# Kernel optimization log

Measured on AMD Instinct MI355X. Metric: run time of the kernel, lower is better.

The kernel has to match this reference:

```python
import jax, jax.numpy as jnp
import numpy as np

INPUT_DIM = 16
BLOCK_LEVELS = 17
OUT_DIM = 5  # dim_weight


def setup_inputs() -> dict:
    key = jax.random.key(0)
    ks = jax.random.split(key, 17)
    B, H, HS = 4096, 1024, 3
    s = 0.05  # keep activations bounded through stacked relu-linears
    return {
        "x": jax.random.normal(ks[0], (B, INPUT_DIM), jnp.float32),
        "Win_f": jax.random.normal(ks[1], (BLOCK_LEVELS, 96, H), jnp.float32) * s,
        "bin_f": jax.random.normal(ks[2], (BLOCK_LEVELS, H), jnp.float32) * s,
        "Win_b": jax.random.normal(ks[3], (BLOCK_LEVELS, 96, H), jnp.float32) * s,
        "bin_b": jax.random.normal(ks[4], (BLOCK_LEVELS, H), jnp.float32) * s,
        "Wblk": jax.random.normal(ks[5], (HS, H, H), jnp.float32) * (s / 2),
        "bblk": jax.random.normal(ks[6], (HS, H), jnp.float32) * s,
        "Wout_f": jax.random.normal(ks[7], (BLOCK_LEVELS, H, OUT_DIM), jnp.float32) * s,
        "bout_f": jax.random.normal(ks[8], (BLOCK_LEVELS, OUT_DIM), jnp.float32) * s,
        "Wout_b": jax.random.normal(ks[9], (BLOCK_LEVELS, H, OUT_DIM), jnp.float32) * s,
        "bout_b": jax.random.normal(ks[10], (BLOCK_LEVELS, OUT_DIM), jnp.float32) * s,
        "W1": jax.random.normal(ks[11], (OUT_DIM, OUT_DIM), jnp.float32) * s,
        "W2": jax.random.normal(ks[12], (OUT_DIM, OUT_DIM), jnp.float32) * s,
        "W3": jax.random.normal(ks[13], (OUT_DIM, OUT_DIM), jnp.float32) * s,
        "W4": jax.random.normal(ks[14], (OUT_DIM * BLOCK_LEVELS, OUT_DIM * BLOCK_LEVELS), jnp.float32) * s,
        "b4": jax.random.normal(ks[15], (OUT_DIM * BLOCK_LEVELS,), jnp.float32) * s,
    }


def _run_direction(x, Win, bin_, Wblk, bblk, Wout, bout):
    # Sequential growing-concat stack: level i takes [x, out_0..out_{i-1}]
    # (width 16 + 5*i). Block weights Wblk are SHARED across all levels.
    outs = []
    prev = x
    for i in range(BLOCK_LEVELS):
        w = Win[i, : INPUT_DIM + OUT_DIM * i, :]  # static slice of padded weight
        h = prev @ w + bin_[i]
        for j in range(Wblk.shape[0]):  # Dropout(p=0) -> Linear -> ReLU
            h = jax.nn.relu(h @ Wblk[j] + bblk[j])
        out = h @ Wout[i] + bout[i]  # (B, 5)
        outs.append(out)
        prev = jnp.concatenate([x] + outs, axis=1)
    return jnp.concatenate(outs, axis=1)  # (B, 85)


def reference(x, Win_f, bin_f, Win_b, bin_b, Wblk, bblk,
              Wout_f, bout_f, Wout_b, bout_b, W1, W2, W3, W4, b4):
    B = x.shape[0]
    tot_f = _run_direction(x, Win_f, bin_f, Wblk, bblk, Wout_f, bout_f)
    tot_b = _run_direction(x, Win_b, bin_b, Wblk, bblk, Wout_b, bout_b)
    tf = tot_f.reshape(B, OUT_DIM, BLOCK_LEVELS)            # (B, 5, 17)
    tb = tot_b.reshape(B, OUT_DIM, BLOCK_LEVELS)[:, :, ::-1]  # reversed levels
    # small attention: q=(B,17,5), k=(B,5,17), v=(B,17,5)
    q = jnp.einsum('bdt,de->bte', tf, W1)
    k = jnp.einsum('bdt,de->bet', tb, W2)
    v = jnp.einsum('bdt,de->bte', tb, W3)
    scores = jnp.einsum('bte,bes->bts', q, k)  # (B, 17, 17)
    attn = jax.nn.softmax(scores, axis=1)      # NB: softmax over dim=1, as in source
    res = jnp.einsum('bts,bse->bte', attn, v)  # (B, 17, 5)
    return res.reshape(B, -1) @ W4 + b4        # (B, 85)
```

## Files before the change

### kernel.cpp

```cpp
#include <hip/hip_runtime.h>
#include <hip/hip_fp16.h>

#define H 1024
#define NLEV 17
#define OD 5
#define TOTD 85
#define PW 128
#define NB 4096

typedef _Float16 half8 __attribute__((ext_vector_type(8)));
typedef float f32x4 __attribute__((ext_vector_type(4)));

__device__ __forceinline__ void g2l16(const void* g, void* l) {
  __builtin_amdgcn_global_load_lds((const __attribute__((address_space(1))) unsigned*)g,
                                   (__attribute__((address_space(3))) unsigned*)l, 16, 0, 0);
}

template<int KSTEPS, bool RELU>
__global__ __launch_bounds__(256, 2)
void gemm_k(const _Float16* __restrict__ A, int ldaB,
            const _Float16* __restrict__ B0, const _Float16* __restrict__ B1, int ldbB,
            const float* __restrict__ bias0, const float* __restrict__ bias1,
            _Float16* __restrict__ C) {
  __shared__ _Float16 sA[128 * 64];
  __shared__ _Float16 sB[128 * 64];
  const int tid = threadIdx.x;
  const int lane = tid & 63;
  const int wave = tid >> 6;
  const int wm = wave >> 1, wn = wave & 1;
  const int mt = blockIdx.x, nt = blockIdx.y;
  const _Float16* Bp = (mt < 32) ? B0 : B1;
  const float* bias = (mt < 32) ? bias0 : bias1;

  char* sAc = (char*)sA;
  char* sBc = (char*)sB;

  const int srow = (lane >> 3);
  const int scb = (lane & 7) << 4;

  f32x4 acc[4][4];
#pragma unroll
  for (int m = 0; m < 4; ++m)
#pragma unroll
    for (int n = 0; n < 4; ++n) acc[m][n] = 0.f;

  const char* Ab = (const char*)A + (size_t)(mt * 128) * ldaB;
  const char* Bb = (const char*)Bp + (size_t)(nt * 128) * ldbB;

  for (int ks = 0; ks < KSTEPS; ++ks) {
    const int kB = ks << 7;
#pragma unroll
    for (int t = 0; t < 4; ++t) {
      int chunk = wave * 4 + t;
      int row = chunk * 8 + srow;
      int off = kB + (scb ^ ((row & 7) << 4));
      g2l16(Ab + (size_t)row * ldaB + off, sAc + chunk * 1024);
      g2l16(Bb + (size_t)row * ldbB + off, sBc + chunk * 1024);
    }
    __syncthreads();
#pragma unroll
    for (int h = 0; h < 2; ++h) {
      half8 af[4], bf[4];
      int kb = h * 64 + ((lane >> 4) << 4);
#pragma unroll
      for (int m = 0; m < 4; ++m) {
        int row = wm * 64 + m * 16 + (lane & 15);
        af[m] = *(const half8*)(sAc + row * 128 + (kb ^ ((row & 7) << 4)));
      }
#pragma unroll
      for (int n = 0; n < 4; ++n) {
        int row = wn * 64 + n * 16 + (lane & 15);
        bf[n] = *(const half8*)(sBc + row * 128 + (kb ^ ((row & 7) << 4)));
      }
#pragma unroll
      for (int m = 0; m < 4; ++m)
#pragma unroll
        for (int n = 0; n < 4; ++n)
          acc[m][n] = __builtin_amdgcn_mfma_f32_16x16x32_f16(af[m], bf[n], acc[m][n], 0, 0, 0);
    }
    __syncthreads();
  }
  const int r0 = mt * 128 + wm * 64 + (lane >> 4) * 4;
#pragma unroll
  for (int n = 0; n < 4; ++n) {
    int col = nt * 128 + wn * 64 + n * 16 + (lane & 15);
    float bv = bias[col];
#pragma unroll
    for (int m = 0; m < 4; ++m) {
      int rbase = r0 + m * 16;
#pragma unroll
      for (int r = 0; r < 4; ++r) {
        float v = acc[m][n][r] + bv;
        if (RELU) v = v > 0.f ? v : 0.f;
        C[(size_t)(rbase + r) * H + col] = (_Float16)v;
      }
    }
  }
}

__global__ __launch_bounds__(256)
void outproj_k(const _Float16* __restrict__ h3,
               const float* __restrict__ Wout_f, const float* __restrict__ Wout_b,
               const float* __restrict__ bout_f, const float* __restrict__ bout_b,
               int lev, float* __restrict__ tot, _Float16* __restrict__ P) {
  int gw = blockIdx.x * 4 + (threadIdx.x >> 6);
  int lane = threadIdx.x & 63;
  int dir = gw >> 12;
  int b = gw & 4095;
  const _Float16* hr = h3 + (size_t)gw * H;
  const float* Wo = (dir ? Wout_b : Wout_f) + (size_t)lev * H * OD;
  const float* bo = (dir ? bout_b : bout_f) + lev * OD;
  float acc[OD] = {0.f, 0.f, 0.f, 0.f, 0.f};
  for (int j = 0; j < 16; ++j) {
    int k = j * 64 + lane;
    float hv = (float)hr[k];
#pragma unroll
    for (int d = 0; d < OD; ++d) acc[d] += hv * Wo[k * OD + d];
  }
#pragma unroll
  for (int off = 32; off; off >>= 1)
#pragma unroll
    for (int d = 0; d < OD; ++d) acc[d] += __shfl_xor(acc[d], off);
  if (lane == 0) {
#pragma unroll
    for (int d = 0; d < OD; ++d) {
      float v = acc[d] + bo[d];
      tot[(size_t)dir * NB * TOTD + (size_t)b * TOTD + lev * OD + d] = v;
      P[((size_t)(dir * NB + b)) * PW + 16 + OD * lev + d] = (_Float16)v;
    }
  }
}

__global__ __launch_bounds__(128)
void attn_k(const float* __restrict__ tot, const float* __restrict__ W1,
            const float* __restrict__ W2, const float* __restrict__ W3,
            const float* __restrict__ W4, const float* __restrict__ b4,
            float* __restrict__ out) {
  __shared__ float tf[5][17], tbr[5][17];
  __shared__ float q[17][5], k2[5][17], vv[17][5];
  __shared__ float sc[17][17];
  __shared__ float res[85];
  int b = blockIdx.x, tid = threadIdx.x;
  const float* tfp = tot + (size_t)b * TOTD;
  const float* tbp = tot + (size_t)NB * TOTD + (size_t)b * TOTD;
  if (tid < 85) {
    int c = tid / 17, t = tid % 17;
    tf[c][t] = tfp[tid];
    tbr[c][t] = tbp[c * 17 + (16 - t)];
  }
  __syncthreads();
  if (tid < 85) {
    int t = tid / 5, e = tid % 5;
    float qa = 0, ka = 0, va = 0;
#pragma unroll
    for (int c = 0; c < 5; ++c) {
      qa += tf[c][t] * W1[c * 5 + e];
      ka += tbr[c][t] * W2[c * 5 + e];
      va += tbr[c][t] * W3[c * 5 + e];
    }
    q[t][e] = qa; k2[e][t] = ka; vv[t][e] = va;
  }
  __syncthreads();
  for (int idx = tid; idx < 289; idx += 128) {
    int t = idx / 17, s = idx % 17;
    float a = 0;
#pragma unroll
    for (int e = 0; e < 5; ++e) a += q[t][e] * k2[e][s];
    sc[t][s] = a;
  }
  __syncthreads();
  if (tid < 17) {
    int s = tid;
    float m = -1e30f;
#pragma unroll
    for (int t = 0; t < 17; ++t) m = fmaxf(m, sc[t][s]);
    float ex[17];
    float sum = 0;
#pragma unroll
    for (int t = 0; t < 17; ++t) { ex[t] = expf(sc[t][s] - m); sum += ex[t]; }
    float inv = 1.f / sum;
#pragma unroll
    for (int t = 0; t < 17; ++t) sc[t][s] = ex[t] * inv;
  }
  __syncthreads();
  if (tid < 85) {
    int t = tid / 5, e = tid % 5;
    float a = 0;
#pragma unroll
    for (int s = 0; s < 17; ++s) a += sc[t][s] * vv[s][e];
    res[tid] = a;
  }
  __syncthreads();
  if (tid < 85) {
    float a = b4[tid];
    for (int s = 0; s < 85; ++s) a += res[s] * W4[s * 85 + tid];
    out[(size_t)b * TOTD + tid] = a;
  }
}

__global__ __launch_bounds__(256)
void prep_wblk(const float* __restrict__ Wblk, _Float16* __restrict__ WblkT) {
  int idx = blockIdx.x * 256 + threadIdx.x;
  int j = idx >> 20;
  int rem = idx & 1048575;
  int n = rem >> 10, k = rem & 1023;
  WblkT[idx] = (_Float16)Wblk[((size_t)j << 20) + ((size_t)k << 10) + n];
}

__global__ __launch_bounds__(256)
void prep_win(const float* __restrict__ Wf, const float* __restrict__ Wb,
              _Float16* __restrict__ WT) {
  int idx = blockIdx.x * 256 + threadIdx.x;
  int d = idx / (17 * 1024 * 128);
  int rem = idx % (17 * 1024 * 128);
  int i = rem / (1024 * 128);
  int r2 = rem % (1024 * 128);
  int n = r2 >> 7, k = r2 & 127;
  const float* W = d ? Wb : Wf;
  WT[idx] = (k < 96) ? (_Float16)W[((size_t)i * 96 + k) * 1024 + n] : (_Float16)0.f;
}

__global__ __launch_bounds__(256)
void prep_p(const float* __restrict__ x, _Float16* __restrict__ P) {
  int idx = blockIdx.x * 256 + threadIdx.x;
  int r = idx >> 7, c = idx & 127;
  int b = r & 4095;
  P[idx] = (c < 16) ? (_Float16)x[b * 16 + c] : (_Float16)0.f;
}

extern "C" void kernel_launch(void* const* d_in, const int* in_sizes, int n_in,
                              void* d_out, int out_size, void* d_ws, size_t ws_size,
                              hipStream_t stream) {
  const float* x = (const float*)d_in[0];
  const float* Win_f = (const float*)d_in[1];
  const float* bin_f = (const float*)d_in[2];
  const float* Win_b = (const float*)d_in[3];
  const float* bin_b = (const float*)d_in[4];
  const float* Wblk = (const float*)d_in[5];
  const float* bblk = (const float*)d_in[6];
  const float* Wout_f = (const float*)d_in[7];
  const float* bout_f = (const float*)d_in[8];
  const float* Wout_b = (const float*)d_in[9];
  const float* bout_b = (const float*)d_in[10];
  const float* W1 = (const float*)d_in[11];
  const float* W2 = (const float*)d_in[12];
  const float* W3 = (const float*)d_in[13];
  const float* W4 = (const float*)d_in[14];
  const float* b4 = (const float*)d_in[15];
  float* out = (float*)d_out;

  char* ws = (char*)d_ws;
  size_t off = 0;
  auto alloc = [&](size_t bytes) {
    void* p = ws + off;
    off += (bytes + 255) & ~(size_t)255;
    return p;
  };
  _Float16* WblkT = (_Float16*)alloc((size_t)3 * 1024 * 1024 * 2);
  _Float16* WinT = (_Float16*)alloc((size_t)2 * 17 * 1024 * 128 * 2);
  _Float16* P = (_Float16*)alloc((size_t)8192 * 128 * 2);
  _Float16* hA = (_Float16*)alloc((size_t)8192 * 1024 * 2);
  _Float16* hB = (_Float16*)alloc((size_t)8192 * 1024 * 2);
  float* tot = (float*)alloc((size_t)2 * NB * TOTD * 4);

  prep_wblk<<<dim3(3 * 1024 * 1024 / 256), dim3(256), 0, stream>>>(Wblk, WblkT);
  prep_win<<<dim3(2 * 17 * 1024 * 128 / 256), dim3(256), 0, stream>>>(Win_f, Win_b, WinT);
  prep_p<<<dim3(8192 * 128 / 256), dim3(256), 0, stream>>>(x, P);

  dim3 ggrid(64, 8), gblk(256);
  for (int i = 0; i < NLEV; ++i) {
    gemm_k<2, false><<<ggrid, gblk, 0, stream>>>(
        P, PW * 2, WinT + (size_t)i * 1024 * 128, WinT + (size_t)(NLEV + i) * 1024 * 128,
        PW * 2, bin_f + i * H, bin_b + i * H, hA);
    gemm_k<16, true><<<ggrid, gblk, 0, stream>>>(
        hA, H * 2, WblkT, WblkT, H * 2, bblk, bblk, hB);
    gemm_k<16, true><<<ggrid, gblk, 0, stream>>>(
        hB, H * 2, WblkT + (1 << 20), WblkT + (1 << 20), H * 2, bblk + H, bblk + H, hA);
    gemm_k<16, true><<<ggrid, gblk, 0, stream>>>(
        hA, H * 2, WblkT + (2 << 20), WblkT + (2 << 20), H * 2, bblk + 2 * H, bblk + 2 * H, hB);
    outproj_k<<<dim3(2048), dim3(256), 0, stream>>>(
        hB, Wout_f, Wout_b, bout_f, bout_b, i, tot, P);
  }
  attn_k<<<dim3(NB), dim3(128), 0, stream>>>(tot, W1, W2, W3, W4, b4, out);
}
```

Measured before the change: 1.556 ms.

## Replace GEMM with 256x128-tile triple-buffered pipelined kernel using 8 waves

Rewrites the MFMA GEMM kernel to use 512-thread blocks computing 256x128 output tiles. The K loop is triple-buffered in LDS with prefetches issued via global_load_lds, and explicit vmcnt waits let loads overlap compute. MFMA issue is interleaved with LDS fragment reads in four quadrants, separated by barriers and raised wave priority. The aim is to hide global-memory latency and reuse the B tile across more rows. The cost is a 144KB LDS footprint, which limits occupancy, plus many barriers per K step.

```diff
diff --git a/kernel.cpp b/kernel.cpp
--- a/kernel.cpp
+++ b/kernel.cpp
@@ -16,27 +16,55 @@
                                    (__attribute__((address_space(3))) unsigned*)l, 16, 0, 0);
 }
 
-template<int KSTEPS, bool RELU>
-__global__ __launch_bounds__(256, 2)
-void gemm_k(const _Float16* __restrict__ A, int ldaB,
-            const _Float16* __restrict__ B0, const _Float16* __restrict__ B1, int ldbB,
-            const float* __restrict__ bias0, const float* __restrict__ bias1,
-            _Float16* __restrict__ C) {
-  __shared__ _Float16 sA[128 * 64];
-  __shared__ _Float16 sB[128 * 64];
+#define BARX() __builtin_amdgcn_s_barrier()
+#define LGKM0() asm volatile("s_waitcnt lgkmcnt(0)" ::: "memory")
+#define VMW0() asm volatile("s_waitcnt vmcnt(0)" ::: "memory")
+#define VMW6() asm volatile("s_waitcnt vmcnt(6)" ::: "memory")
+#define VMW12() asm volatile("s_waitcnt vmcnt(12)" ::: "memory")
+
+#define MM(m, n)                                                                               \
+  acc[m][n] = __builtin_amdgcn_mfma_f32_16x16x32_f16(aF[m][0], bF[n][0], acc[m][n], 0, 0, 0); \
+  acc[m][n] = __builtin_amdgcn_mfma_f32_16x16x32_f16(aF[m][1], bF[n][1], acc[m][n], 0, 0, 0);
+
+#define RDA(m)                                                     \
+  {                                                                \
+    const int row_ = wm * 64 + (m) * 16 + (lane & 15);             \
+    const char* p_ = sAb + row_ * 128;                             \
+    aF[m][0] = *(const half8*)(p_ + (ko ^ swr));                   \
+    aF[m][1] = *(const half8*)(p_ + ((64 | ko) ^ swr));            \
+  }
+#define RDB(n)                                                     \
+  {                                                                \
+    const int row_ = wn * 64 + (n) * 16 + (lane & 15);             \
+    const char* p_ = sBb + row_ * 128;                             \
+    bF[n][0] = *(const half8*)(p_ + (ko ^ swr));                   \
+    bF[n][1] = *(const half8*)(p_ + ((64 | ko) ^ swr));            \
+  }
+
+template<int NT, bool RELU>
+__global__ __launch_bounds__(512, 2)
+void gemm2_k(const _Float16* __restrict__ A, int ldaB,
+             const _Float16* __restrict__ B0, const _Float16* __restrict__ B1, int ldbB,
+             const float* __restrict__ bias0, const float* __restrict__ bias1,
+             _Float16* __restrict__ C) {
+  __shared__ __align__(16) char lds[147456];
+  char* ldsA = lds;
+  char* ldsB = lds + 98304;
   const int tid = threadIdx.x;
   const int lane = tid & 63;
   const int wave = tid >> 6;
-  const int wm = wave >> 1, wn = wave & 1;
-  const int mt = blockIdx.x, nt = blockIdx.y;
-  const _Float16* Bp = (mt < 32) ? B0 : B1;
-  const float* bias = (mt < 32) ? bias0 : bias1;
-
-  char* sAc = (char*)sA;
-  char* sBc = (char*)sB;
-
-  const int srow = (lane >> 3);
-  const int scb = (lane & 7) << 4;
+  const int wm = wave >> 1;
+  const int wn = wave & 1;
+  const int mt = blockIdx.x;
+  const int ntile = blockIdx.y;
+  const _Float16* Bp = (mt < 16) ? B0 : B1;
+  const float* bias = (mt < 16) ? bias0 : bias1;
+  const char* Ab = (const char*)A + (size_t)(mt * 256) * ldaB;
+  const char* Bb = (const char*)Bp + (size_t)(ntile * 128) * ldbB;
+  const int srow = lane >> 3;
+  const int soff = ((lane & 7) << 4) ^ (srow << 4);
+  const int ko = (lane >> 4) << 4;
+  const int swr = (lane & 7) << 4;
 
   f32x4 acc[4][4];
 #pragma unroll
@@ -44,55 +72,76 @@
 #pragma unroll
     for (int n = 0; n < 4; ++n) acc[m][n] = 0.f;
 
-  const char* Ab = (const char*)A + (size_t)(mt * 128) * ldaB;
-  const char* Bb = (const char*)Bp + (size_t)(nt * 128) * ldbB;
-
-  for (int ks = 0; ks < KSTEPS; ++ks) {
-    const int kB = ks << 7;
-#pragma unroll
-    for (int t = 0; t < 4; ++t) {
-      int chunk = wave * 4 + t;
-      int row = chunk * 8 + srow;
-      int off = kB + (scb ^ ((row & 7) << 4));
-      g2l16(Ab + (size_t)row * ldaB + off, sAc + chunk * 1024);
-      g2l16(Bb + (size_t)row * ldbB + off, sBc + chunk * 1024);
-    }
-    __syncthreads();
-#pragma unroll
-    for (int h = 0; h < 2; ++h) {
-      half8 af[4], bf[4];
-      int kb = h * 64 + ((lane >> 4) << 4);
-#pragma unroll
-      for (int m = 0; m < 4; ++m) {
-        int row = wm * 64 + m * 16 + (lane & 15);
-        af[m] = *(const half8*)(sAc + row * 128 + (kb ^ ((row & 7) << 4)));
-      }
-#pragma unroll
-      for (int n = 0; n < 4; ++n) {
-        int row = wn * 64 + n * 16 + (lane & 15);
-        bf[n] = *(const half8*)(sBc + row * 128 + (kb ^ ((row & 7) << 4)));
-      }
-#pragma unroll
-      for (int m = 0; m < 4; ++m)
-#pragma unroll
-        for (int n = 0; n < 4; ++n)
-          acc[m][n] = __builtin_amdgcn_mfma_f32_16x16x32_f16(af[m], bf[n], acc[m][n], 0, 0, 0);
-    }
-    __syncthreads();
-  }
-  const int r0 = mt * 128 + wm * 64 + (lane >> 4) * 4;
+  auto STAGE = [&](int t) {
+    const int b = t % 3;
+    const int kB = t << 7;
+#pragma unroll
+    for (int c = 0; c < 4; ++c) {
+      int chunk = wave * 4 + c;
+      g2l16(Ab + (size_t)(chunk * 8 + srow) * ldaB + kB + soff,
+            ldsA + b * 32768 + chunk * 1024);
+    }
+#pragma unroll
+    for (int c = 0; c < 2; ++c) {
+      int chunk = wave * 2 + c;
+      g2l16(Bb + (size_t)(chunk * 8 + srow) * ldbB + kB + soff,
+            ldsB + b * 16384 + chunk * 1024);
+    }
+  };
+
+  STAGE(0);
+  STAGE(1);
+  if (NT > 2) STAGE(2);
+  if (NT > 2) { VMW12(); } else { VMW6(); }
+  BARX();
+
+#pragma unroll
+  for (int t = 0; t < NT; ++t) {
+    const char* sAb = ldsA + (t % 3) * 32768;
+    const char* sBb = ldsB + (t % 3) * 16384;
+    half8 aF[4][2], bF[4][2];
+    RDA(0); RDA(1); RDB(0); RDB(1);
+    BARX(); LGKM0();
+    __builtin_amdgcn_s_setprio(1);
+    MM(0, 0); MM(0, 1); MM(1, 0); MM(1, 1);
+    __builtin_amdgcn_s_setprio(0);
+    BARX();
+    RDB(2); RDB(3);
+    BARX(); LGKM0();
+    __builtin_amdgcn_s_setprio(1);
+    MM(0, 2); MM(0, 3); MM(1, 2); MM(1, 3);
+    __builtin_amdgcn_s_setprio(0);
+    BARX();
+    RDA(2); RDA(3);
+    BARX(); LGKM0();
+    __builtin_amdgcn_s_setprio(1);
+    MM(2, 0); MM(2, 1); MM(3, 0); MM(3, 1);
+    __builtin_amdgcn_s_setprio(0);
+    BARX();
+    if (t + 3 < NT) STAGE(t + 3);
+    BARX();
+    __builtin_amdgcn_s_setprio(1);
+    MM(2, 2); MM(2, 3); MM(3, 2); MM(3, 3);
+    __builtin_amdgcn_s_setprio(0);
+    if (t < NT - 1) {
+      const int rem = NT - 2 - t;
+      if (rem >= 2) { VMW12(); } else if (rem == 1) { VMW6(); } else { VMW0(); }
+      BARX();
+    }
+  }
+
+  const int r0 = mt * 256 + wm * 64 + ((lane >> 4) << 2);
 #pragma unroll
   for (int n = 0; n < 4; ++n) {
-    int col = nt * 128 + wn * 64 + n * 16 + (lane & 15);
+    int col = ntile * 128 + wn * 64 + n * 16 + (lane & 15);
     float bv = bias[col];
 #pragma unroll
     for (int m = 0; m < 4; ++m) {
-      int rbase = r0 + m * 16;
 #pragma unroll
       for (int r = 0; r < 4; ++r) {
         float v = acc[m][n][r] + bv;
-        if (RELU) v = v > 0.f ? v : 0.f;
-        C[(size_t)(rbase + r) * H + col] = (_Float16)v;
+        if (RELU) v = fmaxf(v, 0.f);
+        C[(size_t)(r0 + m * 16 + r) * H + col] = (_Float16)v;
       }
     }
   }
@@ -232,9 +281,7 @@
                               void* d_out, int out_size, void* d_ws, size_t ws_size,
                               hipStream_t stream) {
   const float* x = (const float*)d_in[0];
-  const float* Win_f = (const float*)d_in[1];
   const float* bin_f = (const float*)d_in[2];
-  const float* Win_b = (const float*)d_in[3];
   const float* bin_b = (const float*)d_in[4];
   const float* Wblk = (const float*)d_in[5];
   const float* bblk = (const float*)d_in[6];
@@ -264,19 +311,20 @@
   float* tot = (float*)alloc((size_t)2 * NB * TOTD * 4);
 
   prep_wblk<<<dim3(3 * 1024 * 1024 / 256), dim3(256), 0, stream>>>(Wblk, WblkT);
-  prep_win<<<dim3(2 * 17 * 1024 * 128 / 256), dim3(256), 0, stream>>>(Win_f, Win_b, WinT);
+  prep_win<<<dim3(2 * 17 * 1024 * 128 / 256), dim3(256), 0, stream>>>(
+      (const float*)d_in[1], (const float*)d_in[3], WinT);
   prep_p<<<dim3(8192 * 128 / 256), dim3(256), 0, stream>>>(x, P);
 
-  dim3 ggrid(64, 8), gblk(256);
+  dim3 ggrid(32, 8), gblk(512);
   for (int i = 0; i < NLEV; ++i) {
-    gemm_k<2, false><<<ggrid, gblk, 0, stream>>>(
+    gemm2_k<2, false><<<ggrid, gblk, 0, stream>>>(
         P, PW * 2, WinT + (size_t)i * 1024 * 128, WinT + (size_t)(NLEV + i) * 1024 * 128,
         PW * 2, bin_f + i * H, bin_b + i * H, hA);
-    gemm_k<16, true><<<ggrid, gblk, 0, stream>>>(
+    gemm2_k<16, true><<<ggrid, gblk, 0, stream>>>(
         hA, H * 2, WblkT, WblkT, H * 2, bblk, bblk, hB);
-    gemm_k<16, true><<<ggrid, gblk, 0, stream>>>(
+    gemm2_k<16, true><<<ggrid, gblk, 0, stream>>>(
         hB, H * 2, WblkT + (1 << 20), WblkT + (1 << 20), H * 2, bblk + H, bblk + H, hA);
-    gemm_k<16, true><<<ggrid, gblk, 0, stream>>>(
+    gemm2_k<16, true><<<ggrid, gblk, 0, stream>>>(
         hA, H * 2, WblkT + (2 << 20), WblkT + (2 << 20), H * 2, bblk + 2 * H, bblk + 2 * H, hB);
     outproj_k<<<dim3(2048), dim3(256), 0, stream>>>(
         hB, Wout_f, Wout_b, bout_f, bout_b, i, tot, P);
```

New measurement: 1.570 ms. No clear change (+0.8%).

## Replace GEMM with 256x128-tile kernel using triple-buffered B and register-resident A

Applied to the files above, without the earlier changes.

Rewrites the fp16 MFMA GEMM so each block computes a 256x128 tile. Each wave holds its 64 A rows directly in registers, loaded from global memory, while B tiles are staged into LDS through a three-deep ring with explicit vmcnt waits and raw barriers. The aim is to overlap global loads with MFMA work and cut LDS traffic and barrier cost. The trade-off is higher register pressure (occupancy drops to 1 block per CU) and a grid half as large, 256 blocks, which may underfill the 256 CUs.

```diff
diff --git a/kernel.cpp b/kernel.cpp
--- a/kernel.cpp
+++ b/kernel.cpp
@@ -16,83 +16,110 @@
                                    (__attribute__((address_space(3))) unsigned*)l, 16, 0, 0);
 }
 
-template<int KSTEPS, bool RELU>
-__global__ __launch_bounds__(256, 2)
-void gemm_k(const _Float16* __restrict__ A, int ldaB,
-            const _Float16* __restrict__ B0, const _Float16* __restrict__ B1, int ldbB,
-            const float* __restrict__ bias0, const float* __restrict__ bias1,
-            _Float16* __restrict__ C) {
-  __shared__ _Float16 sA[128 * 64];
-  __shared__ _Float16 sB[128 * 64];
+#define BARX() __builtin_amdgcn_s_barrier()
+#define VMW0() asm volatile("s_waitcnt vmcnt(0)" ::: "memory")
+#define VMW8() asm volatile("s_waitcnt vmcnt(8)" ::: "memory")
+#define VMW12() asm volatile("s_waitcnt vmcnt(12)" ::: "memory")
+
+template<int NT, bool RELU>
+__global__ __launch_bounds__(256, 1)
+void gemm3_k(const _Float16* __restrict__ A, int ldaB,
+             const _Float16* __restrict__ B0, const _Float16* __restrict__ B1, int ldbB,
+             const float* __restrict__ bias0, const float* __restrict__ bias1,
+             _Float16* __restrict__ C) {
+  __shared__ __align__(16) char ldsB[49152];
   const int tid = threadIdx.x;
   const int lane = tid & 63;
   const int wave = tid >> 6;
-  const int wm = wave >> 1, wn = wave & 1;
-  const int mt = blockIdx.x, nt = blockIdx.y;
-  const _Float16* Bp = (mt < 32) ? B0 : B1;
-  const float* bias = (mt < 32) ? bias0 : bias1;
-
-  char* sAc = (char*)sA;
-  char* sBc = (char*)sB;
-
-  const int srow = (lane >> 3);
-  const int scb = (lane & 7) << 4;
-
-  f32x4 acc[4][4];
+  const int mt = blockIdx.x;
+  const int ntile = blockIdx.y;
+  const _Float16* Bp = (mt < 16) ? B0 : B1;
+  const float* bias = (mt < 16) ? bias0 : bias1;
+  const char* Ab = (const char*)A + (size_t)(mt * 256 + wave * 64) * ldaB;
+  const char* Bb = (const char*)Bp + (size_t)(ntile * 128) * ldbB;
+  const int srow = lane >> 3;
+  const int soff = ((lane & 7) << 4) ^ (srow << 4);
+  const int ko = (lane >> 4) << 4;
+  const int swr = (lane & 7) << 4;
+
+  f32x4 acc[4][8];
 #pragma unroll
   for (int m = 0; m < 4; ++m)
 #pragma unroll
-    for (int n = 0; n < 4; ++n) acc[m][n] = 0.f;
-
-  const char* Ab = (const char*)A + (size_t)(mt * 128) * ldaB;
-  const char* Bb = (const char*)Bp + (size_t)(nt * 128) * ldbB;
-
-  for (int ks = 0; ks < KSTEPS; ++ks) {
-    const int kB = ks << 7;
-#pragma unroll
-    for (int t = 0; t < 4; ++t) {
-      int chunk = wave * 4 + t;
-      int row = chunk * 8 + srow;
-      int off = kB + (scb ^ ((row & 7) << 4));
-      g2l16(Ab + (size_t)row * ldaB + off, sAc + chunk * 1024);
-      g2l16(Bb + (size_t)row * ldbB + off, sBc + chunk * 1024);
-    }
-    __syncthreads();
-#pragma unroll
-    for (int h = 0; h < 2; ++h) {
-      half8 af[4], bf[4];
-      int kb = h * 64 + ((lane >> 4) << 4);
-#pragma unroll
-      for (int m = 0; m < 4; ++m) {
-        int row = wm * 64 + m * 16 + (lane & 15);
-        af[m] = *(const half8*)(sAc + row * 128 + (kb ^ ((row & 7) << 4)));
-      }
-#pragma unroll
-      for (int n = 0; n < 4; ++n) {
-        int row = wn * 64 + n * 16 + (lane & 15);
-        bf[n] = *(const half8*)(sBc + row * 128 + (kb ^ ((row & 7) << 4)));
-      }
+    for (int n = 0; n < 8; ++n) acc[m][n] = 0.f;
+
+  auto STAGEB = [&](int t) {
+    const int b = t % 3;
+    const int kB = t << 7;
+#pragma unroll
+    for (int c = 0; c < 4; ++c) {
+      int chunk = wave * 4 + c;
+      g2l16(Bb + (size_t)(chunk * 8 + srow) * ldbB + kB + soff,
+            ldsB + b * 16384 + chunk * 1024);
+    }
+  };
+  auto LOADA = [&](half8 (*dst)[2], int t) {
+    const int kB = (t << 7) + ko;
+#pragma unroll
+    for (int m = 0; m < 4; ++m) {
+      const char* p = Ab + (size_t)(m * 16 + (lane & 15)) * ldaB + kB;
+      dst[m][0] = *(const half8*)p;
+      dst[m][1] = *(const half8*)(p + 64);
+    }
+  };
+  auto BODY = [&](int t, half8 (*aC)[2]) {
+    const char* sBb = ldsB + (t % 3) * 16384;
+    half8 bF[8];
+#pragma unroll
+    for (int n = 0; n < 8; ++n)
+      bF[n] = *(const half8*)(sBb + (n * 16 + (lane & 15)) * 128 + (ko ^ swr));
+#pragma unroll
+    for (int n = 0; n < 8; ++n)
 #pragma unroll
       for (int m = 0; m < 4; ++m)
-#pragma unroll
-        for (int n = 0; n < 4; ++n)
-          acc[m][n] = __builtin_amdgcn_mfma_f32_16x16x32_f16(af[m], bf[n], acc[m][n], 0, 0, 0);
-    }
-    __syncthreads();
-  }
-  const int r0 = mt * 128 + wm * 64 + (lane >> 4) * 4;
-#pragma unroll
-  for (int n = 0; n < 4; ++n) {
-    int col = nt * 128 + wn * 64 + n * 16 + (lane & 15);
+        acc[m][n] = __builtin_amdgcn_mfma_f32_16x16x32_f16(aC[m][0], bF[n], acc[m][n], 0, 0, 0);
+#pragma unroll
+    for (int n = 0; n < 8; ++n)
+      bF[n] = *(const half8*)(sBb + (n * 16 + (lane & 15)) * 128 + ((64 | ko) ^ swr));
+#pragma unroll
+    for (int n = 0; n < 8; ++n)
+#pragma unroll
+      for (int m = 0; m < 4; ++m)
+        acc[m][n] = __builtin_amdgcn_mfma_f32_16x16x32_f16(aC[m][1], bF[n], acc[m][n], 0, 0, 0);
+    BARX();
+  };
+
+  half8 a0[4][2], a1[4][2];
+  STAGEB(0);
+  LOADA(a0, 0);
+  STAGEB(1);
+  VMW12();
+  BARX();
+
+  int t = 0;
+#pragma unroll 1
+  for (; t + 2 < NT; t += 2) {
+    STAGEB(t + 2); LOADA(a1, t + 1); VMW12(); BODY(t, a0);
+    STAGEB(t + 3); LOADA(a0, t + 2); VMW12(); BODY(t + 1, a1);
+  }
+  LOADA(a1, NT - 1);
+  VMW8();
+  BODY(NT - 2, a0);
+  VMW0();
+  BODY(NT - 1, a1);
+
+  const int r0 = mt * 256 + wave * 64 + ((lane >> 4) << 2);
+#pragma unroll
+  for (int n = 0; n < 8; ++n) {
+    int col = ntile * 128 + n * 16 + (lane & 15);
     float bv = bias[col];
 #pragma unroll
     for (int m = 0; m < 4; ++m) {
-      int rbase = r0 + m * 16;
 #pragma unroll
       for (int r = 0; r < 4; ++r) {
         float v = acc[m][n][r] + bv;
-        if (RELU) v = v > 0.f ? v : 0.f;
-        C[(size_t)(rbase + r) * H + col] = (_Float16)v;
+        if (RELU) v = fmaxf(v, 0.f);
+        C[(size_t)(r0 + m * 16 + r) * H + col] = (_Float16)v;
       }
     }
   }
@@ -232,9 +259,7 @@
                               void* d_out, int out_size, void* d_ws, size_t ws_size,
                               hipStream_t stream) {
   const float* x = (const float*)d_in[0];
-  const float* Win_f = (const float*)d_in[1];
   const float* bin_f = (const float*)d_in[2];
-  const float* Win_b = (const float*)d_in[3];
   const float* bin_b = (const float*)d_in[4];
   const float* Wblk = (const float*)d_in[5];
   const float* bblk = (const float*)d_in[6];
@@ -264,19 +289,20 @@
   float* tot = (float*)alloc((size_t)2 * NB * TOTD * 4);
 
   prep_wblk<<<dim3(3 * 1024 * 1024 / 256), dim3(256), 0, stream>>>(Wblk, WblkT);
-  prep_win<<<dim3(2 * 17 * 1024 * 128 / 256), dim3(256), 0, stream>>>(Win_f, Win_b, WinT);
+  prep_win<<<dim3(2 * 17 * 1024 * 128 / 256), dim3(256), 0, stream>>>(
+      (const float*)d_in[1], (const float*)d_in[3], WinT);
   prep_p<<<dim3(8192 * 128 / 256), dim3(256), 0, stream>>>(x, P);
 
-  dim3 ggrid(64, 8), gblk(256);
+  dim3 ggrid(32, 8), gblk(256);
   for (int i = 0; i < NLEV; ++i) {
-    gemm_k<2, false><<<ggrid, gblk, 0, stream>>>(
+    gemm3_k<2, false><<<ggrid, gblk, 0, stream>>>(
         P, PW * 2, WinT + (size_t)i * 1024 * 128, WinT + (size_t)(NLEV + i) * 1024 * 128,
         PW * 2, bin_f + i * H, bin_b + i * H, hA);
-    gemm_k<16, true><<<ggrid, gblk, 0, stream>>>(
+    gemm3_k<16, true><<<ggrid, gblk, 0, stream>>>(
         hA, H * 2, WblkT, WblkT, H * 2, bblk, bblk, hB);
-    gemm_k<16, true><<<ggrid, gblk, 0, stream>>>(
+    gemm3_k<16, true><<<ggrid, gblk, 0, stream>>>(
         hB, H * 2, WblkT + (1 << 20), WblkT + (1 << 20), H * 2, bblk + H, bblk + H, hA);
-    gemm_k<16, true><<<ggrid, gblk, 0, stream>>>(
+    gemm3_k<16, true><<<ggrid, gblk, 0, stream>>>(
         hA, H * 2, WblkT + (2 << 20), WblkT + (2 << 20), H * 2, bblk + 2 * H, bblk + 2 * H, hB);
     outproj_k<<<dim3(2048), dim3(256), 0, stream>>>(
         hB, Wout_f, Wout_b, bout_f, bout_b, i, tot, P);
```

Result: slower. 1.972 ms (+26.7%).

## Double-buffer GEMM LDS tiles with async prefetch and vectorize outproj loads

Applied to the files above, without the earlier changes.

The GEMM kernel now stages the next K tile into a second LDS buffer while the current one is consumed. It uses partial vmcnt waits, raw barriers and s_setprio around the MFMA section to overlap global-to-LDS copies with compute. The output projection reads hidden rows as 8-wide half vectors instead of scalar halves. The LDS footprint grows to 128KB per block, far more than the two stages need, which limits residency to one block per CU and may halve the concurrent waves for the 512-block grid.

```diff
diff --git a/kernel.cpp b/kernel.cpp
--- a/kernel.cpp
+++ b/kernel.cpp
@@ -16,14 +16,17 @@
                                    (__attribute__((address_space(3))) unsigned*)l, 16, 0, 0);
 }
 
-template<int KSTEPS, bool RELU>
+#define BARX() __builtin_amdgcn_s_barrier()
+#define VMW0() asm volatile("s_waitcnt vmcnt(0)" ::: "memory")
+#define VMW8() asm volatile("s_waitcnt vmcnt(8)" ::: "memory")
+
+template<int NT, bool RELU>
 __global__ __launch_bounds__(256, 2)
-void gemm_k(const _Float16* __restrict__ A, int ldaB,
-            const _Float16* __restrict__ B0, const _Float16* __restrict__ B1, int ldbB,
-            const float* __restrict__ bias0, const float* __restrict__ bias1,
-            _Float16* __restrict__ C) {
-  __shared__ _Float16 sA[128 * 64];
-  __shared__ _Float16 sB[128 * 64];
+void gemm4_k(const _Float16* __restrict__ A, int ldaB,
+             const _Float16* __restrict__ B0, const _Float16* __restrict__ B1, int ldbB,
+             const float* __restrict__ bias0, const float* __restrict__ bias1,
+             _Float16* __restrict__ C) {
+  __shared__ __align__(16) char lds[131072];
   const int tid = threadIdx.x;
   const int lane = tid & 63;
   const int wave = tid >> 6;
@@ -31,68 +34,82 @@
   const int mt = blockIdx.x, nt = blockIdx.y;
   const _Float16* Bp = (mt < 32) ? B0 : B1;
   const float* bias = (mt < 32) ? bias0 : bias1;
-
-  char* sAc = (char*)sA;
-  char* sBc = (char*)sB;
-
-  const int srow = (lane >> 3);
-  const int scb = (lane & 7) << 4;
-
-  f32x4 acc[4][4];
-#pragma unroll
-  for (int m = 0; m < 4; ++m)
-#pragma unroll
-    for (int n = 0; n < 4; ++n) acc[m][n] = 0.f;
-
   const char* Ab = (const char*)A + (size_t)(mt * 128) * ldaB;
   const char* Bb = (const char*)Bp + (size_t)(nt * 128) * ldbB;
 
-  for (int ks = 0; ks < KSTEPS; ++ks) {
-    const int kB = ks << 7;
-#pragma unroll
-    for (int t = 0; t < 4; ++t) {
-      int chunk = wave * 4 + t;
+  const int srow = lane >> 3;
+  const int soff = ((lane & 7) << 4) ^ (srow << 4);
+  const int ko = (lane >> 4) << 4;
+  const int swr = (lane & 7) << 4;
+
+  f32x4 acc[4][4];
+#pragma unroll
+  for (int m = 0; m < 4; ++m)
+#pragma unroll
+    for (int n = 0; n < 4; ++n) acc[m][n] = 0.f;
+
+  auto STAGE = [&](int t) {
+    char* bufA = lds + (t & 1) * 65536;
+    char* bufB = bufA + 32768;
+    const int kB = t << 7;
+#pragma unroll
+    for (int c = 0; c < 4; ++c) {
+      int chunk = wave * 4 + c;
       int row = chunk * 8 + srow;
-      int off = kB + (scb ^ ((row & 7) << 4));
-      g2l16(Ab + (size_t)row * ldaB + off, sAc + chunk * 1024);
-      g2l16(Bb + (size_t)row * ldbB + off, sBc + chunk * 1024);
-    }
-    __syncthreads();
+      g2l16(Ab + (size_t)row * ldaB + kB + soff, bufA + chunk * 1024);
+      g2l16(Bb + (size_t)row * ldbB + kB + soff, bufB + chunk * 1024);
+    }
+  };
+
+  STAGE(0);
+#pragma unroll 1
+  for (int t = 0; t < NT; ++t) {
+    if (t + 1 < NT) {
+      STAGE(t + 1);
+      VMW8();
+    } else {
+      VMW0();
+    }
+    BARX();
+    const char* sAb = lds + (t & 1) * 65536;
+    const char* sBb = sAb + 32768;
+    __builtin_amdgcn_s_setprio(1);
 #pragma unroll
     for (int h = 0; h < 2; ++h) {
-      half8 af[4], bf[4];
-      int kb = h * 64 + ((lane >> 4) << 4);
+      half8 aF[4], bF[4];
+      const int kb = (h << 6) | ko;
 #pragma unroll
       for (int m = 0; m < 4; ++m) {
         int row = wm * 64 + m * 16 + (lane & 15);
-        af[m] = *(const half8*)(sAc + row * 128 + (kb ^ ((row & 7) << 4)));
+        aF[m] = *(const half8*)(sAb + row * 128 + (kb ^ swr));
       }
 #pragma unroll
       for (int n = 0; n < 4; ++n) {
         int row = wn * 64 + n * 16 + (lane & 15);
-        bf[n] = *(const half8*)(sBc + row * 128 + (kb ^ ((row & 7) << 4)));
+        bF[n] = *(const half8*)(sBb + row * 128 + (kb ^ swr));
       }
 #pragma unroll
       for (int m = 0; m < 4; ++m)
 #pragma unroll
         for (int n = 0; n < 4; ++n)
-          acc[m][n] = __builtin_amdgcn_mfma_f32_16x16x32_f16(af[m], bf[n], acc[m][n], 0, 0, 0);
-    }
-    __syncthreads();
-  }
-  const int r0 = mt * 128 + wm * 64 + (lane >> 4) * 4;
+          acc[m][n] = __builtin_amdgcn_mfma_f32_16x16x32_f16(aF[m], bF[n], acc[m][n], 0, 0, 0);
+    }
+    __builtin_amdgcn_s_setprio(0);
+    if (t + 1 < NT) BARX();
+  }
+
+  const int r0 = mt * 128 + wm * 64 + ((lane >> 4) << 2);
 #pragma unroll
   for (int n = 0; n < 4; ++n) {
     int col = nt * 128 + wn * 64 + n * 16 + (lane & 15);
     float bv = bias[col];
 #pragma unroll
     for (int m = 0; m < 4; ++m) {
-      int rbase = r0 + m * 16;
 #pragma unroll
       for (int r = 0; r < 4; ++r) {
         float v = acc[m][n][r] + bv;
-        if (RELU) v = v > 0.f ? v : 0.f;
-        C[(size_t)(rbase + r) * H + col] = (_Float16)v;
+        if (RELU) v = fmaxf(v, 0.f);
+        C[(size_t)(r0 + m * 16 + r) * H + col] = (_Float16)v;
       }
     }
   }
@@ -107,15 +124,21 @@
   int lane = threadIdx.x & 63;
   int dir = gw >> 12;
   int b = gw & 4095;
-  const _Float16* hr = h3 + (size_t)gw * H;
+  const half8* hr8 = (const half8*)(h3 + (size_t)gw * H);
   const float* Wo = (dir ? Wout_b : Wout_f) + (size_t)lev * H * OD;
   const float* bo = (dir ? bout_b : bout_f) + lev * OD;
   float acc[OD] = {0.f, 0.f, 0.f, 0.f, 0.f};
-  for (int j = 0; j < 16; ++j) {
-    int k = j * 64 + lane;
-    float hv = (float)hr[k];
-#pragma unroll
-    for (int d = 0; d < OD; ++d) acc[d] += hv * Wo[k * OD + d];
+#pragma unroll
+  for (int jj = 0; jj < 2; ++jj) {
+    int g = jj * 64 + lane;
+    half8 v = hr8[g];
+#pragma unroll
+    for (int e = 0; e < 8; ++e) {
+      float hv = (float)v[e];
+      int k = g * 8 + e;
+#pragma unroll
+      for (int d = 0; d < OD; ++d) acc[d] += hv * Wo[k * OD + d];
+    }
   }
 #pragma unroll
   for (int off = 32; off; off >>= 1)
@@ -232,9 +255,7 @@
                               void* d_out, int out_size, void* d_ws, size_t ws_size,
                               hipStream_t stream) {
   const float* x = (const float*)d_in[0];
-  const float* Win_f = (const float*)d_in[1];
   const float* bin_f = (const float*)d_in[2];
-  const float* Win_b = (const float*)d_in[3];
   const float* bin_b = (const float*)d_in[4];
   const float* Wblk = (const float*)d_in[5];
   const float* bblk = (const float*)d_in[6];
@@ -264,19 +285,20 @@
   float* tot = (float*)alloc((size_t)2 * NB * TOTD * 4);
 
   prep_wblk<<<dim3(3 * 1024 * 1024 / 256), dim3(256), 0, stream>>>(Wblk, WblkT);
-  prep_win<<<dim3(2 * 17 * 1024 * 128 / 256), dim3(256), 0, stream>>>(Win_f, Win_b, WinT);
+  prep_win<<<dim3(2 * 17 * 1024 * 128 / 256), dim3(256), 0, stream>>>(
+      (const float*)d_in[1], (const float*)d_in[3], WinT);
   prep_p<<<dim3(8192 * 128 / 256), dim3(256), 0, stream>>>(x, P);
 
   dim3 ggrid(64, 8), gblk(256);
   for (int i = 0; i < NLEV; ++i) {
-    gemm_k<2, false><<<ggrid, gblk, 0, stream>>>(
+    gemm4_k<2, false><<<ggrid, gblk, 0, stream>>>(
         P, PW * 2, WinT + (size_t)i * 1024 * 128, WinT + (size_t)(NLEV + i) * 1024 * 128,
         PW * 2, bin_f + i * H, bin_b + i * H, hA);
-    gemm_k<16, true><<<ggrid, gblk, 0, stream>>>(
+    gemm4_k<16, true><<<ggrid, gblk, 0, stream>>>(
         hA, H * 2, WblkT, WblkT, H * 2, bblk, bblk, hB);
-    gemm_k<16, true><<<ggrid, gblk, 0, stream>>>(
+    gemm4_k<16, true><<<ggrid, gblk, 0, stream>>>(
         hB, H * 2, WblkT + (1 << 20), WblkT + (1 << 20), H * 2, bblk + H, bblk + H, hA);
-    gemm_k<16, true><<<ggrid, gblk, 0, stream>>>(
+    gemm4_k<16, true><<<ggrid, gblk, 0, stream>>>(
         hA, H * 2, WblkT + (2 << 20), WblkT + (2 << 20), H * 2, bblk + 2 * H, bblk + 2 * H, hB);
     outproj_k<<<dim3(2048), dim3(256), 0, stream>>>(
         hB, Wout_f, Wout_b, bout_f, bout_b, i, tot, P);
```

After: 1.891 ms. 21.5% more time.
